# Optimization experiments

Measured on AMD Instinct MI355X. Metric: run time of the kernel, lower is better.

Reference implementation:

```python
import jax, jax.numpy as jnp
import numpy as np

H, I, O = 1024, 256, 256
B, T = 64, 512


def _orthogonal(key, rows, cols):
    n = max(rows, cols)
    a = jax.random.normal(key, (n, n), dtype=jnp.float32)
    q, r = jnp.linalg.qr(a)
    q = q * jnp.sign(jnp.diag(r))
    return q[:rows, :cols]


def setup_inputs() -> dict:
    key = jax.random.key(0)
    k0, k1, k2, k3 = jax.random.split(key, 4)
    return {
        "inputs": jax.random.normal(k0, (B, T, I), dtype=jnp.float32),
        "w_rec": _orthogonal(k1, H, H),      # nn.Linear weight [out,in]
        "b_rec": jnp.zeros((H,), jnp.float32),
        "w_in": _orthogonal(k2, H, I),
        "b_in": jnp.zeros((H,), jnp.float32),
        "w_out": _orthogonal(k3, O, H),
        "b_out": jnp.zeros((O,), jnp.float32),
        "scale": jnp.ones((O,), jnp.float32),
        "shift": jnp.zeros((O,), jnp.float32),
    }


def reference(inputs, w_rec, b_rec, w_in, b_in, w_out, b_out, scale, shift):
    # Precompute input projections for all timesteps: [B,T,H]
    x_proj = jnp.einsum('bti,hi->bth', inputs, w_in) + b_in

    def step(h, x_t):
        h_new = jax.nn.relu(h @ w_rec.T + b_rec + x_t)  # [B,H]
        out_t = scale * (h_new @ w_out.T + b_out) - shift  # [B,O]
        return h_new, (out_t, h_new)

    h0 = jnp.zeros((inputs.shape[0], w_rec.shape[0]), inputs.dtype)
    _, (outs, hids) = jax.lax.scan(step, h0, jnp.swapaxes(x_proj, 0, 1))
    # scan stacks along time axis 0 -> [T,B,*]; move to [B,T,*]
    return jnp.swapaxes(outs, 0, 1), jnp.swapaxes(hids, 0, 1)
```

## Files before the change

kernel.cpp:

```cpp
#include <hip/hip_runtime.h>

#define B_ 64
#define T_ 512
#define H_ 1024
#define I_ 256
#define O_ 256

template <int KTOT, int EPI>
__global__ __launch_bounds__(256) void gemm_bt(
    const float* __restrict__ A, const float* __restrict__ Bw,
    const float* __restrict__ bias, const float* __restrict__ scale,
    const float* __restrict__ shift, float* __restrict__ C, int M, int N)
{
    __shared__ float As[64][68];
    __shared__ float Bs[64][68];
    const int tid = threadIdx.x;
    const int tx = tid & 15;
    const int ty = tid >> 4;
    const int NB = N >> 6;
    const int mblk = blockIdx.x / NB;
    const int nblk = blockIdx.x % NB;
    const int m0 = mblk << 6, n0 = nblk << 6;
    const int NC = KTOT / 64;

    float acc[4][4];
#pragma unroll
    for (int i = 0; i < 4; ++i) {
#pragma unroll
        for (int j = 0; j < 4; ++j) acc[i][j] = 0.f;
    }

    float4 ra[4], rb[4];
#pragma unroll
    for (int i = 0; i < 4; ++i) {
        int r = ty + 16 * i;
        ra[i] = *(const float4*)(A + (size_t)(m0 + r) * KTOT + tx * 4);
        rb[i] = *(const float4*)(Bw + (size_t)(n0 + r) * KTOT + tx * 4);
    }

    for (int c = 0; c < NC; ++c) {
#pragma unroll
        for (int i = 0; i < 4; ++i) {
            int r = ty + 16 * i;
            *(float4*)(&As[r][(tx ^ (r >> 2)) * 4]) = ra[i];
            *(float4*)(&Bs[r][(tx ^ (r >> 2)) * 4]) = rb[i];
        }
        __syncthreads();
        if (c + 1 < NC) {
            int kc = (c + 1) * 64;
#pragma unroll
            for (int i = 0; i < 4; ++i) {
                int r = ty + 16 * i;
                ra[i] = *(const float4*)(A + (size_t)(m0 + r) * KTOT + kc + tx * 4);
                rb[i] = *(const float4*)(Bw + (size_t)(n0 + r) * KTOT + kc + tx * 4);
            }
        }
#pragma unroll
        for (int kg = 0; kg < 16; ++kg) {
            float4 a4[4], b4[4];
#pragma unroll
            for (int i = 0; i < 4; ++i)
                a4[i] = *(const float4*)(&As[4 * ty + i][(kg ^ ty) * 4]);
#pragma unroll
            for (int j = 0; j < 4; ++j)
                b4[j] = *(const float4*)(&Bs[4 * tx + j][(kg ^ tx) * 4]);
#pragma unroll
            for (int i = 0; i < 4; ++i) {
#pragma unroll
                for (int j = 0; j < 4; ++j) {
                    acc[i][j] += a4[i].x * b4[j].x + a4[i].y * b4[j].y +
                                 a4[i].z * b4[j].z + a4[i].w * b4[j].w;
                }
            }
        }
        __syncthreads();
    }

    float4 bi4 = *(const float4*)(bias + n0 + tx * 4);
    float4 sc4, sh4;
    if (EPI == 1) {
        sc4 = *(const float4*)(scale + n0 + tx * 4);
        sh4 = *(const float4*)(shift + n0 + tx * 4);
    }
#pragma unroll
    for (int i = 0; i < 4; ++i) {
        float4 r;
        if (EPI == 0) {
            r.x = acc[i][0] + bi4.x;
            r.y = acc[i][1] + bi4.y;
            r.z = acc[i][2] + bi4.z;
            r.w = acc[i][3] + bi4.w;
        } else {
            r.x = sc4.x * (acc[i][0] + bi4.x) - sh4.x;
            r.y = sc4.y * (acc[i][1] + bi4.y) - sh4.y;
            r.z = sc4.z * (acc[i][2] + bi4.z) - sh4.z;
            r.w = sc4.w * (acc[i][3] + bi4.w) - sh4.w;
        }
        *(float4*)(C + (size_t)(m0 + 4 * ty + i) * N + n0 + 4 * tx) = r;
    }
}

__global__ __launch_bounds__(256) void rnn_rec(
    const float* __restrict__ w_rec, const float* __restrict__ b_rec,
    float* __restrict__ hids, unsigned* __restrict__ flags)
{
    __shared__ float Wl[16 * 1024];
    __shared__ float Hl[16 * 1024];
    const int tid = threadIdx.x;
    const int bid = blockIdx.x;
    const int xcd = bid & 7;
    const int dom = xcd >> 1;
    const int wg  = ((xcd & 1) << 5) | (bid >> 3);
    const int r0 = wg << 4;
    const int b0 = dom << 4;
    unsigned* fl_dom = flags + (dom << 11);
    unsigned* fl_own = fl_dom + (wg << 5);

    {
        const int r = tid >> 4, l = tid & 15;
        const float* src = w_rec + (size_t)(r0 + r) * H_;
        float* dst = Wl + r * 1024;
#pragma unroll
        for (int u = 0; u < 16; ++u) {
            int kg = u * 16 + l;
            float4 v = *(const float4*)(src + kg * 4);
            int pk = kg ^ ((kg >> 3) & 7) ^ ((r >> 3) << 2);
            *(float4*)(dst + pk * 4) = v;
        }
    }

    const int bl_e = tid >> 4, rl_e = tid & 15;
    const float brec = b_rec[r0 + rl_e];
    float* xcell = hids + ((size_t)(b0 + bl_e) * T_) * H_ + (r0 + rl_e);

    const int ks = tid >> 3;
    const int rb = (tid >> 2) & 1;
    const int bb = tid & 3;
    const int cW = (ks & 7) ^ (rb << 2);
    const int cH = (ks & 7) ^ (bb << 1);
    const int rd_idx = tid ^ (((tid >> 6) & 3) << 3);

    __syncthreads();

    for (int t = 0; t < T_; ++t) {
        float x = __hip_atomic_load(&xcell[(size_t)t * H_], __ATOMIC_RELAXED,
                                    __HIP_MEMORY_SCOPE_AGENT);
        float sum = 0.f;
        if (t > 0) {
            if (tid < 64) {
                long long ts = __builtin_amdgcn_s_memrealtime();
                for (;;) {
                    unsigned f = __hip_atomic_load(fl_dom + (tid << 5),
                                                   __ATOMIC_RELAXED,
                                                   __HIP_MEMORY_SCOPE_AGENT);
                    if (__all(f >= (unsigned)t)) break;
                    if (__builtin_amdgcn_s_memrealtime() - ts > 10000000LL) break;
                }
            }
            __syncthreads();

            {
                const int blr = tid >> 4, l = tid & 15;
                const float* hsrc = hids + ((size_t)(b0 + blr) * T_ + (t - 1)) * H_;
                float* hdst = Hl + blr * 1024;
#pragma unroll
                for (int u = 0; u < 16; ++u) {
                    int kg = u * 16 + l;
                    float4 v = *(const float4*)(hsrc + kg * 4);
                    int pk = kg ^ ((kg >> 3) & 7) ^ ((blr >> 2) << 1);
                    *(float4*)(hdst + pk * 4) = v;
                }
            }
            __syncthreads();

            float acc[4][8];
#pragma unroll
            for (int i = 0; i < 4; ++i) {
#pragma unroll
                for (int j = 0; j < 8; ++j) acc[i][j] = 0.f;
            }
#pragma unroll
            for (int j4 = 0; j4 < 8; ++j4) {
                const int sW = (j4 ^ cW) << 2;
                const int sH = (j4 ^ cH) << 2;
                float4 hv[4], wv[8];
#pragma unroll
                for (int i = 0; i < 4; ++i)
                    hv[i] = *(const float4*)(Hl + (bb * 4 + i) * 1024 + ks * 32 + sH);
#pragma unroll
                for (int i = 0; i < 8; ++i)
                    wv[i] = *(const float4*)(Wl + (rb * 8 + i) * 1024 + ks * 32 + sW);
#pragma unroll
                for (int bi = 0; bi < 4; ++bi) {
#pragma unroll
                    for (int ri = 0; ri < 8; ++ri) {
                        acc[bi][ri] += hv[bi].x * wv[ri].x + hv[bi].y * wv[ri].y +
                                       hv[bi].z * wv[ri].z + hv[bi].w * wv[ri].w;
                    }
                }
            }
            __syncthreads();

            float* scr = Hl;
#pragma unroll
            for (int bi = 0; bi < 4; ++bi) {
#pragma unroll
                for (int ri = 0; ri < 8; ++ri) {
                    int o = ((bb * 4 + bi) * 16 + rb * 8 + ri) ^ (bb << 3);
                    scr[ks * 259 + o] = acc[bi][ri];
                }
            }
            __syncthreads();
            float s0 = 0.f, s1 = 0.f, s2 = 0.f, s3 = 0.f;
#pragma unroll
            for (int s = 0; s < 8; ++s) {
                s0 += scr[(4 * s + 0) * 259 + rd_idx];
                s1 += scr[(4 * s + 1) * 259 + rd_idx];
                s2 += scr[(4 * s + 2) * 259 + rd_idx];
                s3 += scr[(4 * s + 3) * 259 + rd_idx];
            }
            sum = (s0 + s1) + (s2 + s3);
        }

        float hnew = fmaxf(sum + brec + x, 0.f);
        __hip_atomic_store(&xcell[(size_t)t * H_], hnew, __ATOMIC_RELAXED,
                           __HIP_MEMORY_SCOPE_AGENT);

        asm volatile("s_waitcnt vmcnt(0)" ::: "memory");
        __syncthreads();
        if (tid == 0)
            __hip_atomic_store(fl_own, (unsigned)(t + 1), __ATOMIC_RELAXED,
                               __HIP_MEMORY_SCOPE_AGENT);
    }
}

extern "C" void kernel_launch(void* const* d_in, const int* in_sizes, int n_in,
                              void* d_out, int out_size, void* d_ws, size_t ws_size,
                              hipStream_t stream)
{
    const float* inputs = (const float*)d_in[0];
    const float* w_rec  = (const float*)d_in[1];
    const float* b_rec  = (const float*)d_in[2];
    const float* w_in   = (const float*)d_in[3];
    const float* b_in   = (const float*)d_in[4];
    const float* w_out  = (const float*)d_in[5];
    const float* b_out  = (const float*)d_in[6];
    const float* scale  = (const float*)d_in[7];
    const float* shift  = (const float*)d_in[8];

    float* outs = (float*)d_out;
    float* hids = outs + (size_t)B_ * T_ * O_;
    unsigned* flags = (unsigned*)d_ws;

    hipMemsetAsync(d_ws, 0, 32768, stream);

    gemm_bt<I_, 0><<<dim3((B_ * T_ / 64) * (H_ / 64)), dim3(256), 0, stream>>>(
        inputs, w_in, b_in, nullptr, nullptr, hids, B_ * T_, H_);

    rnn_rec<<<dim3(256), dim3(256), 0, stream>>>(w_rec, b_rec, hids, flags);

    gemm_bt<H_, 1><<<dim3((B_ * T_ / 64) * (O_ / 64)), dim3(256), 0, stream>>>(
        hids, w_out, b_out, scale, shift, outs, B_ * T_, O_);
}
```

Measured before the change: 4.574 ms.

## Let each wave poll its own flag subset and gather its own hidden-state slice

Each of the four waves now polls a 16-flag subset of the domain barrier flags, and afterwards loads exactly the hidden-state slice it will write into shared memory. This removes the block-wide __syncthreads between polling and the gather, so waves can start loading as soon as their own producers are done. The hidden-state store becomes an atomic exchange whose returned value is consumed, presumably so the write is acknowledged before the flag is published. This trades a barrier for more complex per-wave visibility reasoning, and the exchange may cost more than a plain store.

```diff
diff --git a/kernel.cpp b/kernel.cpp
--- a/kernel.cpp
+++ b/kernel.cpp
@@ -140,6 +140,12 @@
     const int cH = (ks & 7) ^ (bb << 1);
     const int rd_idx = tid ^ (((tid >> 6) & 3) << 3);
 
+    const int wv = tid >> 6;
+    const int lane = tid & 63;
+    const int kgS = (wv << 6) | lane;
+    const int pk0 = kgS ^ ((kgS >> 3) & 7);
+    const unsigned* fl_poll = fl_dom + (((wv << 4) | (lane & 15)) << 5);
+
     __syncthreads();
 
     for (int t = 0; t < T_; ++t) {
@@ -147,28 +153,23 @@
                                     __HIP_MEMORY_SCOPE_AGENT);
         float sum = 0.f;
         if (t > 0) {
-            if (tid < 64) {
+            {
                 long long ts = __builtin_amdgcn_s_memrealtime();
                 for (;;) {
-                    unsigned f = __hip_atomic_load(fl_dom + (tid << 5),
-                                                   __ATOMIC_RELAXED,
+                    unsigned f = __hip_atomic_load(fl_poll, __ATOMIC_RELAXED,
                                                    __HIP_MEMORY_SCOPE_AGENT);
                     if (__all(f >= (unsigned)t)) break;
                     if (__builtin_amdgcn_s_memrealtime() - ts > 10000000LL) break;
                 }
             }
-            __syncthreads();
 
             {
-                const int blr = tid >> 4, l = tid & 15;
-                const float* hsrc = hids + ((size_t)(b0 + blr) * T_ + (t - 1)) * H_;
-                float* hdst = Hl + blr * 1024;
+                const float* hs = hids + ((size_t)b0 * T_ + (t - 1)) * H_ + (kgS << 2);
 #pragma unroll
                 for (int u = 0; u < 16; ++u) {
-                    int kg = u * 16 + l;
-                    float4 v = *(const float4*)(hsrc + kg * 4);
-                    int pk = kg ^ ((kg >> 3) & 7) ^ ((blr >> 2) << 1);
-                    *(float4*)(hdst + pk * 4) = v;
+                    float4 v = *(const float4*)(hs + (size_t)u * T_ * H_);
+                    int pk = pk0 ^ ((u >> 2) << 1);
+                    *(float4*)(Hl + u * 1024 + pk * 4) = v;
                 }
             }
             __syncthreads();
@@ -183,19 +184,19 @@
             for (int j4 = 0; j4 < 8; ++j4) {
                 const int sW = (j4 ^ cW) << 2;
                 const int sH = (j4 ^ cH) << 2;
-                float4 hv[4], wv[8];
+                float4 hv[4], wv8[8];
 #pragma unroll
                 for (int i = 0; i < 4; ++i)
                     hv[i] = *(const float4*)(Hl + (bb * 4 + i) * 1024 + ks * 32 + sH);
 #pragma unroll
                 for (int i = 0; i < 8; ++i)
-                    wv[i] = *(const float4*)(Wl + (rb * 8 + i) * 1024 + ks * 32 + sW);
+                    wv8[i] = *(const float4*)(Wl + (rb * 8 + i) * 1024 + ks * 32 + sW);
 #pragma unroll
                 for (int bi = 0; bi < 4; ++bi) {
 #pragma unroll
                     for (int ri = 0; ri < 8; ++ri) {
-                        acc[bi][ri] += hv[bi].x * wv[ri].x + hv[bi].y * wv[ri].y +
-                                       hv[bi].z * wv[ri].z + hv[bi].w * wv[ri].w;
+                        acc[bi][ri] += hv[bi].x * wv8[ri].x + hv[bi].y * wv8[ri].y +
+                                       hv[bi].z * wv8[ri].z + hv[bi].w * wv8[ri].w;
                     }
                 }
             }
@@ -223,8 +224,10 @@
         }
 
         float hnew = fmaxf(sum + brec + x, 0.f);
-        __hip_atomic_store(&xcell[(size_t)t * H_], hnew, __ATOMIC_RELAXED,
-                           __HIP_MEMORY_SCOPE_AGENT);
+        float old = __hip_atomic_exchange(&xcell[(size_t)t * H_], hnew,
+                                          __ATOMIC_RELAXED,
+                                          __HIP_MEMORY_SCOPE_AGENT);
+        asm volatile("" :: "v"(old));
 
         asm volatile("s_waitcnt vmcnt(0)" ::: "memory");
         __syncthreads();
```

Result: faster. 4.403 ms (-3.7%).
